# Kernel tuning notes

Hardware: AMD Instinct MI355X
Metric: run time of the kernel (lower is better)

The kernel has to match this reference:

```python
import jax, jax.numpy as jnp
import numpy as np

N, IN_DIM, HEADS, OUT_DIM = 4096, 128, 4, 64
NEG_INF = -9.0e15  # finite mask value, matches torch source


def setup_inputs() -> dict:
    key = jax.random.key(0)
    k1, k2, k3, k4, k5 = jax.random.split(key, 5)
    x = jax.random.normal(k1, (N, IN_DIM), dtype=jnp.float32)
    adj_mask = jax.random.bernoulli(k2, 0.1, (N, N))  # bool, j->i edges
    # xavier-uniform-ish scales
    lim_w = float(np.sqrt(6.0 / (IN_DIM + HEADS * OUT_DIM)))
    W_lin = jax.random.uniform(k3, (IN_DIM, HEADS * OUT_DIM), minval=-lim_w, maxval=lim_w, dtype=jnp.float32)
    lim_a = float(np.sqrt(6.0 / (2 * OUT_DIM + 1)))
    a_src = jax.random.uniform(k4, (OUT_DIM,), minval=-lim_a, maxval=lim_a, dtype=jnp.float32)
    a_dst = jax.random.uniform(k5, (OUT_DIM,), minval=-lim_a, maxval=lim_a, dtype=jnp.float32)
    return {"x": x, "adj_mask": adj_mask, "W_lin": W_lin, "a_src": a_src, "a_dst": a_dst}


def reference(x, adj_mask, W_lin, a_src, a_dst):
    n = x.shape[0]
    h = (x @ W_lin).reshape(n, HEADS, OUT_DIM)           # (N, H, D)
    # att(cat(h_i, h_j)) decomposes linearly: a_src.h_i + a_dst.h_j
    s_i = jnp.einsum("nhd,d->nh", h, a_src)              # (N, H) contribution of dest node i
    s_j = jnp.einsum("nhd,d->nh", h, a_dst)              # (N, H) contribution of source node j
    e = jax.nn.leaky_relu(s_i[:, None, :] + s_j[None, :, :], 0.2)  # (N, N, H)
    e = jnp.where(adj_mask[:, :, None], e, NEG_INF)
    attn = jax.nn.softmax(e, axis=1)                     # softmax over source nodes j
    out = jnp.einsum("ijh,jhd->ihd", attn, h)            # per-head aggregation
    return out.reshape(n, HEADS * OUT_DIM)               # concat=True
```

## Files before the change

### kernel.cpp

```cpp
#include <hip/hip_runtime.h>
#include <math.h>


#define N 4096
#define IN_DIM 128
#define HEADS 4
#define OUT_DIM 64
#define HD 256
#define LOG2E 1.4426950408889634f
#define PSHIFT 8.0f

typedef _Float16 f16x8 __attribute__((ext_vector_type(8)));
typedef __fp16 fp16x2 __attribute__((ext_vector_type(2)));
typedef float f32x4 __attribute__((ext_vector_type(4)));

union F16x8u { fp16x2 h2[4]; f16x8 v; };

#define WS_HB_OFF    0u
#define WS_SSRC_OFF  2097152u
#define WS_SDT_OFF   2162688u
#define WS_BITT_OFF  2228224u
#define WS_HSUMP_OFF 4325376u

__device__ __forceinline__ unsigned pack_bytes(unsigned v) {
  return (v & 1u) | ((v >> 7) & 2u) | ((v >> 14) & 4u) | ((v >> 21) & 8u);
}

__global__ __launch_bounds__(256) void prep_k(const void* __restrict__ mraw,
                                              unsigned* __restrict__ bits_t,
                                              const float* __restrict__ x,
                                              const float* __restrict__ W,
                                              const float* __restrict__ a_src,
                                              const float* __restrict__ a_dst,
                                              _Float16* __restrict__ hb,
                                              float* __restrict__ s_src,
                                              float* __restrict__ s_dst_t,
                                              float* __restrict__ hsum_part) {
  if (blockIdx.x < 2048) {
    __shared__ int s_flag;
    if (threadIdx.x == 0) s_flag = 0;
    __syncthreads();
    const unsigned* mw = (const unsigned*)mraw;
    int bad = 0, g = 0;
    for (int i = threadIdx.x; i < 1024; i += 256) {
      unsigned v = mw[i];
      if (v & 0xFEFEFEFEu) bad = 1;
      if (v > 1u) g = 1;
    }
    if (bad || g) atomicOr(&s_flag, (bad ? 1 : 0) | (g ? 2 : 0));
    __syncthreads();
    const bool byte_fmt = ((s_flag & 1) == 0) && ((s_flag & 2) != 0);

    int w = blockIdx.x * 256 + threadIdx.x;
    unsigned ob = 0u;
    if (byte_fmt) {
      const uint4* p = (const uint4*)((const unsigned char*)mraw + (size_t)w * 32u);
      uint4 a = p[0], b = p[1];
      ob  =  pack_bytes(a.x)        | (pack_bytes(a.y) << 4)  | (pack_bytes(a.z) << 8)  | (pack_bytes(a.w) << 12);
      ob |= (pack_bytes(b.x) << 16) | (pack_bytes(b.y) << 20) | (pack_bytes(b.z) << 24) | (pack_bytes(b.w) << 28);
    } else {
      const uint4* p = (const uint4*)((const unsigned*)mraw + (size_t)w * 32u);
#pragma unroll
      for (int k = 0; k < 8; ++k) {
        uint4 v = p[k];
        ob |= (v.x ? 1u : 0u) << (4 * k);
        ob |= (v.y ? 1u : 0u) << (4 * k + 1);
        ob |= (v.z ? 1u : 0u) << (4 * k + 2);
        ob |= (v.w ? 1u : 0u) << (4 * k + 3);
      }
    }
    const int row = w >> 7, jc = w & 127;
    bits_t[((size_t)(row >> 6) * 128 + jc) * 64 + (row & 63)] = ob;
  } else {
    __shared__ float xs[8][IN_DIM];
    const int blk = blockIdx.x - 2048;
    const int i0 = blk * 8;
    const int c = threadIdx.x;

    ((float4*)&xs[0][0])[c] = ((const float4*)(x + (size_t)i0 * IN_DIM))[c];
    __syncthreads();

    float acc[8];
#pragma unroll
    for (int r = 0; r < 8; ++r) acc[r] = 0.f;

    for (int kk = 0; kk < IN_DIM / 4; ++kk) {
      const int k = kk * 4;
      float w0 = W[(size_t)(k + 0) * HD + c];
      float w1 = W[(size_t)(k + 1) * HD + c];
      float w2 = W[(size_t)(k + 2) * HD + c];
      float w3 = W[(size_t)(k + 3) * HD + c];
#pragma unroll
      for (int r = 0; r < 8; ++r) {
        float4 xv = *(const float4*)(&xs[r][k]);
        acc[r] = fmaf(xv.x, w0, fmaf(xv.y, w1, fmaf(xv.z, w2, fmaf(xv.w, w3, acc[r]))));
      }
    }

    {
      const int head = c >> 6, nt = (c >> 4) & 3, m15 = c & 15;
      const int unit = (head * 128 + (i0 >> 5)) * 4 + nt;
      const int lanep = ((i0 & 31) >> 3) * 16 + m15;
      f16x8 v;
#pragma unroll
      for (int r = 0; r < 8; ++r) v[r] = (_Float16)acc[r];
      *(f16x8*)(hb + (size_t)unit * 512 + lanep * 8) = v;
    }

    {
      float loc = 0.f;
#pragma unroll
      for (int r = 0; r < 8; ++r) loc += acc[r];
      hsum_part[(size_t)blk * HD + c] = loc;
    }

    const int hw = c >> 6, lane = c & 63;
    const float as = a_src[lane], ad = a_dst[lane];
#pragma unroll
    for (int r = 0; r < 8; ++r) {
      float vs = acc[r] * as, vd = acc[r] * ad;
#pragma unroll
      for (int off = 1; off < 64; off <<= 1) {
        vs += __shfl_xor(vs, off);
        vd += __shfl_xor(vd, off);
      }
      if (lane == 0) {
        s_src[(size_t)(i0 + r) * HEADS + hw] = vs * LOG2E;
        s_dst_t[(size_t)hw * N + (i0 + r)] = vd * LOG2E;
      }
    }
  }
}

__global__ __launch_bounds__(512, 4) void gat_fused(const _Float16* __restrict__ hb,
                                                    const float* __restrict__ s_src,
                                                    const float* __restrict__ s_dst_t,
                                                    const unsigned* __restrict__ bits_t,
                                                    const float* __restrict__ hsum_part,
                                                    float4* __restrict__ out) {
  __shared__ float red[8][32][64];
  __shared__ float lred[8][32];

  const int tid = threadIdx.x;
  const int w = tid >> 6;
  const int lane = tid & 63;
  const int m15 = lane & 15;
  const int quad = lane >> 4;
  const int head = blockIdx.x >> 7;
  const int rb = blockIdx.x & 127;
  const int i0 = rb * 32;
  const int rA = i0 + m15;
  const int rB = rA + 16;

  const float siA = s_src[(size_t)rA * HEADS + head];
  const float siB = s_src[(size_t)rB * HEADS + head];
  const float siAa = siA - PSHIFT, siAb = 0.2f * siA - PSHIFT;
  const float siBa = siB - PSHIFT, siBb = 0.2f * siB - PSHIFT;

  const unsigned* mt = bits_t + ((size_t)(rb >> 1) * 128 + w * 16) * 64 + (i0 & 32) + m15;
  const float* sjb = s_dst_t + (size_t)head * N + w * 512 + quad * 8;
  const _Float16* hbp = hb + ((size_t)(head * 128 + w * 16) * 4) * 512 + lane * 8;

  f32x4 accA0 = {0.f, 0.f, 0.f, 0.f}, accA1 = accA0, accA2 = accA0, accA3 = accA0;
  f32x4 accB0 = accA0, accB1 = accA0, accB2 = accA0, accB3 = accA0;
  float lA = 0.f, lB = 0.f;

  const int shq = quad * 8;

  for (int c = 0; c < 16; ++c) {
    const unsigned mwA = mt[c * 64];
    const unsigned mwB = mt[c * 64 + 16];
    const float4 sa = *(const float4*)(sjb + c * 32);
    const float4 sb = *(const float4*)(sjb + c * 32 + 4);

    const f16x8 b0 = *(const f16x8*)(hbp + (size_t)(c * 4 + 0) * 512);
    const f16x8 b1 = *(const f16x8*)(hbp + (size_t)(c * 4 + 1) * 512);
    const f16x8 b2 = *(const f16x8*)(hbp + (size_t)(c * 4 + 2) * 512);
    const f16x8 b3 = *(const f16x8*)(hbp + (size_t)(c * 4 + 3) * 512);

    const unsigned wA = mwA >> shq;
    const unsigned wB = mwB >> shq;
    const float sjs[8] = {sa.x, sa.y, sa.z, sa.w, sb.x, sb.y, sb.z, sb.w};

    F16x8u uA, uB;
#pragma unroll
    for (int t2 = 0; t2 < 4; ++t2) {
      float pA[2], pB[2];
#pragma unroll
      for (int q = 0; q < 2; ++q) {
        const int t = t2 * 2 + q;
        const float sj = sjs[t];
        const float mA = fmaxf(siAa + sj, fmaf(0.2f, sj, siAb));
        const float mB = fmaxf(siBa + sj, fmaf(0.2f, sj, siBb));
        const float xA = (((wA >> t) & 1u) ? mA : -1.0e38f);
        const float xB = (((wB >> t) & 1u) ? mB : -1.0e38f);
        pA[q] = __builtin_amdgcn_exp2f(xA);
        pB[q] = __builtin_amdgcn_exp2f(xB);
        lA += pA[q];
        lB += pB[q];
      }
      uA.h2[t2] = __builtin_amdgcn_cvt_pkrtz(pA[0], pA[1]);
      uB.h2[t2] = __builtin_amdgcn_cvt_pkrtz(pB[0], pB[1]);
    }

    accA0 = __builtin_amdgcn_mfma_f32_16x16x32_f16(uA.v, b0, accA0, 0, 0, 0);
    accA1 = __builtin_amdgcn_mfma_f32_16x16x32_f16(uA.v, b1, accA1, 0, 0, 0);
    accA2 = __builtin_amdgcn_mfma_f32_16x16x32_f16(uA.v, b2, accA2, 0, 0, 0);
    accA3 = __builtin_amdgcn_mfma_f32_16x16x32_f16(uA.v, b3, accA3, 0, 0, 0);
    accB0 = __builtin_amdgcn_mfma_f32_16x16x32_f16(uB.v, b0, accB0, 0, 0, 0);
    accB1 = __builtin_amdgcn_mfma_f32_16x16x32_f16(uB.v, b1, accB1, 0, 0, 0);
    accB2 = __builtin_amdgcn_mfma_f32_16x16x32_f16(uB.v, b2, accB2, 0, 0, 0);
    accB3 = __builtin_amdgcn_mfma_f32_16x16x32_f16(uB.v, b3, accB3, 0, 0, 0);
  }

  lA += __shfl_xor(lA, 16); lA += __shfl_xor(lA, 32);
  lB += __shfl_xor(lB, 16); lB += __shfl_xor(lB, 32);
  if (quad == 0) {
    lred[w][m15] = lA;
    lred[w][16 + m15] = lB;
  }

#pragma unroll
  for (int reg = 0; reg < 4; ++reg) {
    const int ra = quad * 4 + reg;
    red[w][ra][m15 +  0] = accA0[reg];
    red[w][ra][m15 + 16] = accA1[reg];
    red[w][ra][m15 + 32] = accA2[reg];
    red[w][ra][m15 + 48] = accA3[reg];
    red[w][16 + ra][m15 +  0] = accB0[reg];
    red[w][16 + ra][m15 + 16] = accB1[reg];
    red[w][16 + ra][m15 + 32] = accB2[reg];
    red[w][16 + ra][m15 + 48] = accB3[reg];
  }
  __syncthreads();

  const int row = tid >> 4;
  const int c4 = tid & 15;
  float4 o = {0.f, 0.f, 0.f, 0.f};
  float lt = 0.f;
#pragma unroll
  for (int k = 0; k < 8; ++k) {
    const float4 v = *(const float4*)&red[k][row][c4 * 4];
    o.x += v.x; o.y += v.y; o.z += v.z; o.w += v.w;
    lt += lred[k][row];
  }
  if (lt == 0.f) {
    float4 hs = {0.f, 0.f, 0.f, 0.f};
    for (int b = 0; b < 512; ++b) {
      float4 t4 = ((const float4*)hsum_part)[(size_t)b * 64 + head * 16 + c4];
      hs.x += t4.x; hs.y += t4.y; hs.z += t4.z; hs.w += t4.w;
    }
    const float cst = 1.0f / (float)N;
    o.x = hs.x * cst; o.y = hs.y * cst; o.z = hs.z * cst; o.w = hs.w * cst;
  } else {
    const float inv = 1.0f / lt;
    o.x *= inv; o.y *= inv; o.z *= inv; o.w *= inv;
  }
  out[(size_t)(i0 + row) * 64 + head * 16 + c4] = o;
}

extern "C" void kernel_launch(void* const* d_in, const int* in_sizes, int n_in,
                              void* d_out, int out_size, void* d_ws, size_t ws_size,
                              hipStream_t stream) {
  (void)in_sizes; (void)n_in; (void)out_size; (void)ws_size;
  const float* x = (const float*)d_in[0];
  const void* mask = d_in[1];
  const float* W = (const float*)d_in[2];
  const float* a_src = (const float*)d_in[3];
  const float* a_dst = (const float*)d_in[4];
  float* out = (float*)d_out;

  char* ws = (char*)d_ws;
  _Float16* hb = (_Float16*)(ws + WS_HB_OFF);
  float* s_src = (float*)(ws + WS_SSRC_OFF);
  float* s_dst_t = (float*)(ws + WS_SDT_OFF);
  unsigned* bits_t = (unsigned*)(ws + WS_BITT_OFF);
  float* hsum_part = (float*)(ws + WS_HSUMP_OFF);

  prep_k<<<2048 + N / 8, 256, 0, stream>>>(mask, bits_t, x, W, a_src, a_dst,
                                           hb, s_src, s_dst_t, hsum_part);
  gat_fused<<<512, 512, 0, stream>>>(hb, s_src, s_dst_t, bits_t, hsum_part,
                                     (float4*)out);
}
```

Before: 141.0 us.

## Double rows per block and compute softmax denominators with ones-MFMA

Each block now uses 1024 threads and covers 64 destination rows per head instead of 32. Two 32-row wave groups share the same source-node slices of h, so those loads are reused within a block. The per-row softmax denominator is now accumulated by an extra MFMA against a vector of ones, replacing the VALU adds and cross-lane shuffles. The LDS reduction buffer grows and is padded to 68 columns to avoid bank conflicts. The trade-off is more MFMA work per chunk, large LDS use, and one block per CU across 256 blocks, which may cut occupancy and latency hiding.

```diff
diff --git a/kernel.cpp b/kernel.cpp
--- a/kernel.cpp
+++ b/kernel.cpp
@@ -132,23 +132,25 @@
   }
 }
 
-__global__ __launch_bounds__(512, 4) void gat_fused(const _Float16* __restrict__ hb,
-                                                    const float* __restrict__ s_src,
-                                                    const float* __restrict__ s_dst_t,
-                                                    const unsigned* __restrict__ bits_t,
-                                                    const float* __restrict__ hsum_part,
-                                                    float4* __restrict__ out) {
-  __shared__ float red[8][32][64];
-  __shared__ float lred[8][32];
+__global__ __launch_bounds__(1024, 4) void gat_fused(const _Float16* __restrict__ hb,
+                                                     const float* __restrict__ s_src,
+                                                     const float* __restrict__ s_dst_t,
+                                                     const unsigned* __restrict__ bits_t,
+                                                     const float* __restrict__ hsum_part,
+                                                     float4* __restrict__ out) {
+  __shared__ float red[8][64][68];
+  __shared__ float lred[8][64];
 
   const int tid = threadIdx.x;
-  const int w = tid >> 6;
+  const int wv = tid >> 6;
+  const int js = wv & 7;
+  const int mg = wv >> 3;
   const int lane = tid & 63;
   const int m15 = lane & 15;
   const int quad = lane >> 4;
-  const int head = blockIdx.x >> 7;
-  const int rb = blockIdx.x & 127;
-  const int i0 = rb * 32;
+  const int head = blockIdx.x >> 6;
+  const int rb = blockIdx.x & 63;
+  const int i0 = rb * 64 + mg * 32;
   const int rA = i0 + m15;
   const int rB = rA + 16;
 
@@ -157,13 +159,17 @@
   const float siAa = siA - PSHIFT, siAb = 0.2f * siA - PSHIFT;
   const float siBa = siB - PSHIFT, siBb = 0.2f * siB - PSHIFT;
 
-  const unsigned* mt = bits_t + ((size_t)(rb >> 1) * 128 + w * 16) * 64 + (i0 & 32) + m15;
-  const float* sjb = s_dst_t + (size_t)head * N + w * 512 + quad * 8;
-  const _Float16* hbp = hb + ((size_t)(head * 128 + w * 16) * 4) * 512 + lane * 8;
+  const unsigned* mt = bits_t + ((size_t)rb * 128 + js * 16) * 64 + mg * 32 + m15;
+  const float* sjb = s_dst_t + (size_t)head * N + js * 512 + quad * 8;
+  const _Float16* hbp = hb + ((size_t)(head * 128 + js * 16) * 4) * 512 + lane * 8;
 
   f32x4 accA0 = {0.f, 0.f, 0.f, 0.f}, accA1 = accA0, accA2 = accA0, accA3 = accA0;
   f32x4 accB0 = accA0, accB1 = accA0, accB2 = accA0, accB3 = accA0;
-  float lA = 0.f, lB = 0.f;
+  f32x4 accLA = accA0, accLB = accA0;
+
+  f16x8 onesv;
+#pragma unroll
+  for (int t = 0; t < 8; ++t) onesv[t] = (_Float16)1.0f;
 
   const int shq = quad * 8;
 
@@ -196,13 +202,13 @@
         const float xB = (((wB >> t) & 1u) ? mB : -1.0e38f);
         pA[q] = __builtin_amdgcn_exp2f(xA);
         pB[q] = __builtin_amdgcn_exp2f(xB);
-        lA += pA[q];
-        lB += pB[q];
       }
       uA.h2[t2] = __builtin_amdgcn_cvt_pkrtz(pA[0], pA[1]);
       uB.h2[t2] = __builtin_amdgcn_cvt_pkrtz(pB[0], pB[1]);
     }
 
+    accLA = __builtin_amdgcn_mfma_f32_16x16x32_f16(uA.v, onesv, accLA, 0, 0, 0);
+    accLB = __builtin_amdgcn_mfma_f32_16x16x32_f16(uB.v, onesv, accLB, 0, 0, 0);
     accA0 = __builtin_amdgcn_mfma_f32_16x16x32_f16(uA.v, b0, accA0, 0, 0, 0);
     accA1 = __builtin_amdgcn_mfma_f32_16x16x32_f16(uA.v, b1, accA1, 0, 0, 0);
     accA2 = __builtin_amdgcn_mfma_f32_16x16x32_f16(uA.v, b2, accA2, 0, 0, 0);
@@ -213,24 +219,25 @@
     accB3 = __builtin_amdgcn_mfma_f32_16x16x32_f16(uB.v, b3, accB3, 0, 0, 0);
   }
 
-  lA += __shfl_xor(lA, 16); lA += __shfl_xor(lA, 32);
-  lB += __shfl_xor(lB, 16); lB += __shfl_xor(lB, 32);
-  if (quad == 0) {
-    lred[w][m15] = lA;
-    lred[w][16 + m15] = lB;
+  if (m15 == 0) {
+#pragma unroll
+    for (int reg = 0; reg < 4; ++reg) {
+      lred[js][mg * 32 + quad * 4 + reg] = accLA[reg];
+      lred[js][mg * 32 + 16 + quad * 4 + reg] = accLB[reg];
+    }
   }
 
 #pragma unroll
   for (int reg = 0; reg < 4; ++reg) {
-    const int ra = quad * 4 + reg;
-    red[w][ra][m15 +  0] = accA0[reg];
-    red[w][ra][m15 + 16] = accA1[reg];
-    red[w][ra][m15 + 32] = accA2[reg];
-    red[w][ra][m15 + 48] = accA3[reg];
-    red[w][16 + ra][m15 +  0] = accB0[reg];
-    red[w][16 + ra][m15 + 16] = accB1[reg];
-    red[w][16 + ra][m15 + 32] = accB2[reg];
-    red[w][16 + ra][m15 + 48] = accB3[reg];
+    const int ra = mg * 32 + quad * 4 + reg;
+    red[js][ra][m15 +  0] = accA0[reg];
+    red[js][ra][m15 + 16] = accA1[reg];
+    red[js][ra][m15 + 32] = accA2[reg];
+    red[js][ra][m15 + 48] = accA3[reg];
+    red[js][16 + ra][m15 +  0] = accB0[reg];
+    red[js][16 + ra][m15 + 16] = accB1[reg];
+    red[js][16 + ra][m15 + 32] = accB2[reg];
+    red[js][16 + ra][m15 + 48] = accB3[reg];
   }
   __syncthreads();
 
@@ -256,7 +263,7 @@
     const float inv = 1.0f / lt;
     o.x *= inv; o.y *= inv; o.z *= inv; o.w *= inv;
   }
-  out[(size_t)(i0 + row) * 64 + head * 16 + c4] = o;
+  out[(size_t)(rb * 64 + row) * 64 + head * 16 + c4] = o;
 }
 
 extern "C" void kernel_launch(void* const* d_in, const int* in_sizes, int n_in,
@@ -279,6 +286,6 @@
 
   prep_k<<<2048 + N / 8, 256, 0, stream>>>(mask, bits_t, x, W, a_src, a_dst,
                                            hb, s_src, s_dst_t, hsum_part);
-  gat_fused<<<512, 512, 0, stream>>>(hb, s_src, s_dst_t, bits_t, hsum_part,
-                                     (float4*)out);
-}
+  gat_fused<<<256, 1024, 0, stream>>>(hb, s_src, s_dst_t, bits_t, hsum_part,
+                                      (float4*)out);
+}
```

New measurement: 140.2 us. About the same (-0.5%).
